# Kernel tuning notes

Measured on AMD Instinct MI355X. Metric: run time of the kernel, lower is better.

Reference implementation:

```python
import jax, jax.numpy as jnp
import numpy as np

def setup_inputs() -> dict:
    key = jax.random.key(0)
    kq, kk, kv = jax.random.split(key, 3)
    B, H, N, D = 2, 12, 4096, 64
    Q = jax.random.normal(kq, (B, H, N, D), dtype=jnp.float32)
    K = jax.random.normal(kk, (B, H, N, D), dtype=jnp.float32)
    V = jax.random.normal(kv, (B, H, N, D), dtype=jnp.float32)
    mask = jnp.ones((B, N), dtype=jnp.float32)
    return {"Q": Q, "K": K, "V": V, "mask": mask}

def reference(Q, K, V, mask):
    # Q, K, V: [B, H, N, D]; mask: [B, N]
    N = Q.shape[2]
    scale = 1.0 / jnp.sqrt(jnp.sqrt(jnp.float32(N)))  # N^(-1/4)
    m = mask[:, None, :, None]                         # [B,1,N,1]
    Qf = (jax.nn.elu(Q) + 1.0) * scale                 # feature map on queries
    Kf = (jax.nn.elu(K) + 1.0) * m * scale             # feature map + mask on keys
    Vm = V * m
    # linear attention: Q (K^T V), contracting over sequence first -> [B,H,D,D]
    KtV = jnp.einsum('bhnd,bhne->bhde', Kf, Vm)
    X = jnp.einsum('bhnd,bhde->bhne', Qf, KtV)
    return X
```

## Files before the change

kernel.cpp:

```cpp
#include <hip/hip_runtime.h>
#include <hip/hip_bf16.h>
#include <math.h>


#define BH_TOT 24
#define NROWS 4096
#define DD 64

typedef __attribute__((ext_vector_type(8))) short bf16x8;
typedef __attribute__((ext_vector_type(4))) float f32x4;

__device__ __forceinline__ float elu1(float x) {
    return x > 0.0f ? x + 1.0f : __expf(x);
}
__device__ __forceinline__ short f2bf(float x) {
    __hip_bfloat16 h = __float2bfloat16(x);
    return *reinterpret_cast<short*>(&h);
}

__global__ __launch_bounds__(128) void la_pass1(
        const float* __restrict__ K, const float* __restrict__ V,
        const float* __restrict__ mask, float* __restrict__ partial,
        float scale, int chunksPerWave) {
    const int bh   = blockIdx.x;
    const int slab = blockIdx.y;
    const int wave = threadIdx.x >> 6;
    const int lane = threadIdx.x & 63;
    const int g = lane >> 4, rg = g * 8, cl = lane & 15;

    const float* __restrict__ Kp = K + (size_t)bh * NROWS * DD;
    const float* __restrict__ Vp = V + (size_t)bh * NROWS * DD;
    const float* __restrict__ mp = mask + (size_t)(bh / 12) * NROWS;

    f32x4 acc[4][4];
#pragma unroll
    for (int i = 0; i < 4; ++i)
#pragma unroll
        for (int j = 0; j < 4; ++j) acc[i][j] = (f32x4)0.0f;

    const int rowsPerBlock = chunksPerWave * 64;
    const int n0 = slab * rowsPerBlock + wave * chunksPerWave * 32;

#pragma unroll 1
    for (int c = 0; c < chunksPerWave; ++c) {
        const int nb = n0 + c * 32 + rg;
        const float* kb = Kp + (size_t)nb * DD + cl;
        const float* vb = Vp + (size_t)nb * DD + cl;
        float mrow[8], kr[8][4], vr[8][4];
#pragma unroll
        for (int jj = 0; jj < 8; ++jj) {
            mrow[jj] = mp[nb + jj];
#pragma unroll
            for (int i = 0; i < 4; ++i) {
                kr[jj][i] = kb[jj * DD + i * 16];
                vr[jj][i] = vb[jj * DD + i * 16];
            }
        }
        bf16x8 af[4], bv[4];
#pragma unroll
        for (int i = 0; i < 4; ++i)
#pragma unroll
            for (int jj = 0; jj < 8; ++jj) {
                af[i][jj] = f2bf(elu1(kr[jj][i]) * (mrow[jj] * scale));
                bv[i][jj] = f2bf(vr[jj][i] * mrow[jj]);
            }
#pragma unroll
        for (int i = 0; i < 4; ++i)
#pragma unroll
            for (int j = 0; j < 4; ++j)
                acc[i][j] = __builtin_amdgcn_mfma_f32_16x16x32_bf16(
                                af[i], bv[j], acc[i][j], 0, 0, 0);
    }

    __shared__ float red[DD * 66];
#define RIDX(i, r, j) ((16 * (i) + 4 * g + (r)) * 66 + 16 * (j) + cl)
    if (wave == 1) {
#pragma unroll
        for (int i = 0; i < 4; ++i)
#pragma unroll
            for (int j = 0; j < 4; ++j)
#pragma unroll
                for (int r = 0; r < 4; ++r) red[RIDX(i, r, j)] = acc[i][j][r];
    }
    __syncthreads();
    if (wave == 0) {
        float* out = partial + ((size_t)bh * gridDim.y + slab) * (DD * DD);
#pragma unroll
        for (int i = 0; i < 4; ++i)
#pragma unroll
            for (int j = 0; j < 4; ++j)
#pragma unroll
                for (int r = 0; r < 4; ++r)
                    out[(16 * i + 4 * g + r) * DD + 16 * j + cl]
                        = acc[i][j][r] + red[RIDX(i, r, j)];
    }
#undef RIDX
}

__global__ __launch_bounds__(256) void la_pass2(
        const float* __restrict__ partial, __hip_bfloat16* __restrict__ ktvT,
        int nw) {
    const int bh = blockIdx.x;
    const int f4 = blockIdx.y * 256 + threadIdx.x;
    const f32x4* base = (const f32x4*)(partial + (size_t)bh * nw * DD * DD) + f4;
    f32x4 s = (f32x4)0.0f;
#pragma unroll 8
    for (int w = 0; w < nw; ++w)
        s += base[(size_t)w * (DD * DD / 4)];
    const int d = f4 >> 4, e0 = (f4 & 15) * 4;
    __hip_bfloat16* o = ktvT + (size_t)bh * DD * DD + d;
#pragma unroll
    for (int q = 0; q < 4; ++q)
        o[(size_t)(e0 + q) * DD] = __float2bfloat16(s[q]);
}

__global__ __launch_bounds__(256) void la_pass3(
        const float* __restrict__ Q, const __hip_bfloat16* __restrict__ ktvT,
        float* __restrict__ X, float scale) {
    const int bh   = blockIdx.x;
    const int wave = threadIdx.x >> 6;
    const int lane = threadIdx.x & 63;
    const int n0   = blockIdx.y * 128 + wave * 32;
    const int rg   = (lane >> 4) * 8;
    const int cl   = lane & 15;

    bf16x8 bfr[2][4];
#pragma unroll
    for (int c2 = 0; c2 < 2; ++c2)
#pragma unroll
        for (int j = 0; j < 4; ++j) {
            const __hip_bfloat16* p = ktvT + (size_t)bh * DD * DD
                                      + (size_t)(16 * j + cl) * DD + 32 * c2 + rg;
            bfr[c2][j] = *reinterpret_cast<const bf16x8*>(p);
        }

    const float* Qp = Q + (size_t)bh * NROWS * DD;
    bf16x8 afr[2][2];
#pragma unroll
    for (int i = 0; i < 2; ++i)
#pragma unroll
        for (int c2 = 0; c2 < 2; ++c2) {
            const float* qp = Qp + (size_t)(n0 + 16 * i + cl) * DD + 32 * c2 + rg;
            float4 q0 = ((const float4*)qp)[0];
            float4 q1 = ((const float4*)qp)[1];
            bf16x8 a;
            a[0] = f2bf(elu1(q0.x) * scale); a[1] = f2bf(elu1(q0.y) * scale);
            a[2] = f2bf(elu1(q0.z) * scale); a[3] = f2bf(elu1(q0.w) * scale);
            a[4] = f2bf(elu1(q1.x) * scale); a[5] = f2bf(elu1(q1.y) * scale);
            a[6] = f2bf(elu1(q1.z) * scale); a[7] = f2bf(elu1(q1.w) * scale);
            afr[i][c2] = a;
        }

    f32x4 acc[2][4];
#pragma unroll
    for (int i = 0; i < 2; ++i)
#pragma unroll
        for (int j = 0; j < 4; ++j) acc[i][j] = (f32x4)0.0f;

#pragma unroll
    for (int i = 0; i < 2; ++i)
#pragma unroll
        for (int j = 0; j < 4; ++j) {
            acc[i][j] = __builtin_amdgcn_mfma_f32_16x16x32_bf16(
                            afr[i][0], bfr[0][j], acc[i][j], 0, 0, 0);
            acc[i][j] = __builtin_amdgcn_mfma_f32_16x16x32_bf16(
                            afr[i][1], bfr[1][j], acc[i][j], 0, 0, 0);
        }

    float* Xp = X + (size_t)bh * NROWS * DD;
#pragma unroll
    for (int i = 0; i < 2; ++i)
#pragma unroll
        for (int j = 0; j < 4; ++j)
#pragma unroll
            for (int r = 0; r < 4; ++r)
                Xp[(size_t)(n0 + 16 * i + (lane >> 4) * 4 + r) * DD + 16 * j + cl]
                    = acc[i][j][r];
}

extern "C" void kernel_launch(void* const* d_in, const int* in_sizes, int n_in,
                              void* d_out, int out_size, void* d_ws, size_t ws_size,
                              hipStream_t stream) {
    const float* Q    = (const float*)d_in[0];
    const float* K    = (const float*)d_in[1];
    const float* V    = (const float*)d_in[2];
    const float* mask = (const float*)d_in[3];
    float* X = (float*)d_out;

    const float scale = 0.125f;

    int slabs = 32;
    while (slabs > 4 &&
           (size_t)BH_TOT * slabs * DD * DD * 4 + (size_t)BH_TOT * DD * DD * 2 > ws_size)
        slabs >>= 1;
    const int chunksPerWave = NROWS / (slabs * 64);

    float* partial = (float*)d_ws;
    __hip_bfloat16* ktvT =
        (__hip_bfloat16*)((char*)d_ws + (size_t)BH_TOT * slabs * DD * DD * 4);

    la_pass1<<<dim3(BH_TOT, slabs), 128, 0, stream>>>(K, V, mask, partial,
                                                      scale, chunksPerWave);
    la_pass2<<<dim3(BH_TOT, 4), 256, 0, stream>>>(partial, ktvT, slabs);
    la_pass3<<<dim3(BH_TOT, 32), 256, 0, stream>>>(Q, ktvT, X, scale);
}
```

Before: 34.23 us.

## Fuse partial reduction into pass1 via last-block atomic counter; vectorize pass3 stores

Merges the separate reduction kernel into the first pass: each block atomically bumps a per-head counter, and the last block to finish sums all slab partials and writes the bf16 K^T V matrix directly. It also swaps the MFMA operand order so the reduced matrix is stored transposed with vectorized writes, and pass3 is restructured so each lane stores contiguous float4 outputs. This removes one kernel launch but adds a memset, threadfences and a serialized tail reduction done by one block per head. The slab count is now fixed and no longer adapts to workspace size.

```diff
diff --git a/kernel.cpp b/kernel.cpp
--- a/kernel.cpp
+++ b/kernel.cpp
@@ -6,6 +6,7 @@
 #define BH_TOT 24
 #define NROWS 4096
 #define DD 64
+#define SLABS 32
 
 typedef __attribute__((ext_vector_type(8))) short bf16x8;
 typedef __attribute__((ext_vector_type(4))) float f32x4;
@@ -18,9 +19,10 @@
     return *reinterpret_cast<short*>(&h);
 }
 
-__global__ __launch_bounds__(128) void la_pass1(
+__global__ __launch_bounds__(128) void la_p12(
         const float* __restrict__ K, const float* __restrict__ V,
         const float* __restrict__ mask, float* __restrict__ partial,
+        __hip_bfloat16* __restrict__ ktvT, int* __restrict__ cnt,
         float scale, int chunksPerWave) {
     const int bh   = blockIdx.x;
     const int slab = blockIdx.y;
@@ -38,8 +40,7 @@
 #pragma unroll
         for (int j = 0; j < 4; ++j) acc[i][j] = (f32x4)0.0f;
 
-    const int rowsPerBlock = chunksPerWave * 64;
-    const int n0 = slab * rowsPerBlock + wave * chunksPerWave * 32;
+    const int n0 = slab * chunksPerWave * 64 + wave * chunksPerWave * 32;
 
 #pragma unroll 1
     for (int c = 0; c < chunksPerWave; ++c) {
@@ -65,82 +66,89 @@
                 bv[i][jj] = f2bf(vr[jj][i] * mrow[jj]);
             }
 #pragma unroll
-        for (int i = 0; i < 4; ++i)
-#pragma unroll
-            for (int j = 0; j < 4; ++j)
-                acc[i][j] = __builtin_amdgcn_mfma_f32_16x16x32_bf16(
-                                af[i], bv[j], acc[i][j], 0, 0, 0);
+        for (int je = 0; je < 4; ++je)
+#pragma unroll
+            for (int id = 0; id < 4; ++id)
+                acc[je][id] = __builtin_amdgcn_mfma_f32_16x16x32_bf16(
+                                  bv[je], af[id], acc[je][id], 0, 0, 0);
     }
 
     __shared__ float red[DD * 66];
-#define RIDX(i, r, j) ((16 * (i) + 4 * g + (r)) * 66 + 16 * (j) + cl)
+    __shared__ int lastFlag;
+#define RIDX(je, r, id) ((16 * (je) + 4 * g + (r)) * 66 + 16 * (id) + cl)
     if (wave == 1) {
 #pragma unroll
-        for (int i = 0; i < 4; ++i)
-#pragma unroll
-            for (int j = 0; j < 4; ++j)
-#pragma unroll
-                for (int r = 0; r < 4; ++r) red[RIDX(i, r, j)] = acc[i][j][r];
+        for (int je = 0; je < 4; ++je)
+#pragma unroll
+            for (int id = 0; id < 4; ++id)
+#pragma unroll
+                for (int r = 0; r < 4; ++r) red[RIDX(je, r, id)] = acc[je][id][r];
     }
     __syncthreads();
     if (wave == 0) {
-        float* out = partial + ((size_t)bh * gridDim.y + slab) * (DD * DD);
-#pragma unroll
-        for (int i = 0; i < 4; ++i)
-#pragma unroll
-            for (int j = 0; j < 4; ++j)
+        float* out = partial + ((size_t)bh * SLABS + slab) * (DD * DD);
+#pragma unroll
+        for (int je = 0; je < 4; ++je)
+#pragma unroll
+            for (int id = 0; id < 4; ++id)
 #pragma unroll
                 for (int r = 0; r < 4; ++r)
-                    out[(16 * i + 4 * g + r) * DD + 16 * j + cl]
-                        = acc[i][j][r] + red[RIDX(i, r, j)];
+                    out[(16 * je + 4 * g + r) * DD + 16 * id + cl]
+                        = acc[je][id][r] + red[RIDX(je, r, id)];
     }
 #undef RIDX
-}
-
-__global__ __launch_bounds__(256) void la_pass2(
-        const float* __restrict__ partial, __hip_bfloat16* __restrict__ ktvT,
-        int nw) {
-    const int bh = blockIdx.x;
-    const int f4 = blockIdx.y * 256 + threadIdx.x;
-    const f32x4* base = (const f32x4*)(partial + (size_t)bh * nw * DD * DD) + f4;
-    f32x4 s = (f32x4)0.0f;
+    __syncthreads();
+
+    if (threadIdx.x == 0) {
+        __threadfence();
+        int old = atomicAdd(&cnt[bh], 1);
+        lastFlag = (old == SLABS - 1) ? 1 : 0;
+    }
+    __syncthreads();
+    if (lastFlag) {
+        __threadfence();
+        const f32x4* base = (const f32x4*)(partial + (size_t)bh * SLABS * DD * DD);
+        __hip_bfloat16* ko = ktvT + (size_t)bh * DD * DD;
+#pragma unroll
+        for (int p = 0; p < 8; ++p) {
+            const int idx = threadIdx.x + p * 128;
+            f32x4 s = (f32x4)0.0f;
 #pragma unroll 8
-    for (int w = 0; w < nw; ++w)
-        s += base[(size_t)w * (DD * DD / 4)];
-    const int d = f4 >> 4, e0 = (f4 & 15) * 4;
-    __hip_bfloat16* o = ktvT + (size_t)bh * DD * DD + d;
-#pragma unroll
-    for (int q = 0; q < 4; ++q)
-        o[(size_t)(e0 + q) * DD] = __float2bfloat16(s[q]);
-}
-
-__global__ __launch_bounds__(256) void la_pass3(
+            for (int w = 0; w < SLABS; ++w)
+                s += base[(size_t)w * (DD * DD / 4) + idx];
+            const int e = idx >> 4, d0 = (idx & 15) * 4;
+            ushort4 u;
+            u.x = (unsigned short)f2bf(s[0]); u.y = (unsigned short)f2bf(s[1]);
+            u.z = (unsigned short)f2bf(s[2]); u.w = (unsigned short)f2bf(s[3]);
+            *reinterpret_cast<ushort4*>(ko + (size_t)e * DD + d0) = u;
+        }
+    }
+}
+
+__global__ __launch_bounds__(256) void la_p3(
         const float* __restrict__ Q, const __hip_bfloat16* __restrict__ ktvT,
         float* __restrict__ X, float scale) {
     const int bh   = blockIdx.x;
     const int wave = threadIdx.x >> 6;
     const int lane = threadIdx.x & 63;
     const int n0   = blockIdx.y * 128 + wave * 32;
-    const int rg   = (lane >> 4) * 8;
-    const int cl   = lane & 15;
-
-    bf16x8 bfr[2][4];
-#pragma unroll
-    for (int c2 = 0; c2 < 2; ++c2)
-#pragma unroll
-        for (int j = 0; j < 4; ++j) {
-            const __hip_bfloat16* p = ktvT + (size_t)bh * DD * DD
-                                      + (size_t)(16 * j + cl) * DD + 32 * c2 + rg;
-            bfr[c2][j] = *reinterpret_cast<const bf16x8*>(p);
-        }
+    const int g = lane >> 4, rg = g * 8, cl = lane & 15;
+
+    bf16x8 afr[4][2];
+#pragma unroll
+    for (int i = 0; i < 4; ++i)
+#pragma unroll
+        for (int c2 = 0; c2 < 2; ++c2)
+            afr[i][c2] = *reinterpret_cast<const bf16x8*>(
+                ktvT + (size_t)bh * DD * DD + (size_t)(16 * i + cl) * DD + 32 * c2 + rg);
 
     const float* Qp = Q + (size_t)bh * NROWS * DD;
-    bf16x8 afr[2][2];
-#pragma unroll
-    for (int i = 0; i < 2; ++i)
+    bf16x8 bfr[2][2];
+#pragma unroll
+    for (int t = 0; t < 2; ++t)
 #pragma unroll
         for (int c2 = 0; c2 < 2; ++c2) {
-            const float* qp = Qp + (size_t)(n0 + 16 * i + cl) * DD + 32 * c2 + rg;
+            const float* qp = Qp + (size_t)(n0 + 16 * t + cl) * DD + 32 * c2 + rg;
             float4 q0 = ((const float4*)qp)[0];
             float4 q1 = ((const float4*)qp)[1];
             bf16x8 a;
@@ -148,34 +156,35 @@
             a[2] = f2bf(elu1(q0.z) * scale); a[3] = f2bf(elu1(q0.w) * scale);
             a[4] = f2bf(elu1(q1.x) * scale); a[5] = f2bf(elu1(q1.y) * scale);
             a[6] = f2bf(elu1(q1.z) * scale); a[7] = f2bf(elu1(q1.w) * scale);
-            afr[i][c2] = a;
-        }
-
-    f32x4 acc[2][4];
-#pragma unroll
-    for (int i = 0; i < 2; ++i)
-#pragma unroll
-        for (int j = 0; j < 4; ++j) acc[i][j] = (f32x4)0.0f;
-
-#pragma unroll
-    for (int i = 0; i < 2; ++i)
-#pragma unroll
-        for (int j = 0; j < 4; ++j) {
-            acc[i][j] = __builtin_amdgcn_mfma_f32_16x16x32_bf16(
-                            afr[i][0], bfr[0][j], acc[i][j], 0, 0, 0);
-            acc[i][j] = __builtin_amdgcn_mfma_f32_16x16x32_bf16(
-                            afr[i][1], bfr[1][j], acc[i][j], 0, 0, 0);
+            bfr[t][c2] = a;
+        }
+
+    f32x4 acc[4][2];
+#pragma unroll
+    for (int i = 0; i < 4; ++i)
+#pragma unroll
+        for (int t = 0; t < 2; ++t) acc[i][t] = (f32x4)0.0f;
+
+#pragma unroll
+    for (int i = 0; i < 4; ++i)
+#pragma unroll
+        for (int t = 0; t < 2; ++t) {
+            acc[i][t] = __builtin_amdgcn_mfma_f32_16x16x32_bf16(
+                            afr[i][0], bfr[t][0], acc[i][t], 0, 0, 0);
+            acc[i][t] = __builtin_amdgcn_mfma_f32_16x16x32_bf16(
+                            afr[i][1], bfr[t][1], acc[i][t], 0, 0, 0);
         }
 
     float* Xp = X + (size_t)bh * NROWS * DD;
 #pragma unroll
-    for (int i = 0; i < 2; ++i)
-#pragma unroll
-        for (int j = 0; j < 4; ++j)
-#pragma unroll
-            for (int r = 0; r < 4; ++r)
-                Xp[(size_t)(n0 + 16 * i + (lane >> 4) * 4 + r) * DD + 16 * j + cl]
-                    = acc[i][j][r];
+    for (int i = 0; i < 4; ++i)
+#pragma unroll
+        for (int t = 0; t < 2; ++t) {
+            float4 v = make_float4(acc[i][t][0], acc[i][t][1],
+                                   acc[i][t][2], acc[i][t][3]);
+            *reinterpret_cast<float4*>(
+                Xp + (size_t)(n0 + 16 * t + cl) * DD + 16 * i + 4 * g) = v;
+        }
 }
 
 extern "C" void kernel_launch(void* const* d_in, const int* in_sizes, int n_in,
@@ -189,18 +198,14 @@
 
     const float scale = 0.125f;
 
-    int slabs = 32;
-    while (slabs > 4 &&
-           (size_t)BH_TOT * slabs * DD * DD * 4 + (size_t)BH_TOT * DD * DD * 2 > ws_size)
-        slabs >>= 1;
-    const int chunksPerWave = NROWS / (slabs * 64);
-
-    float* partial = (float*)d_ws;
-    __hip_bfloat16* ktvT =
-        (__hip_bfloat16*)((char*)d_ws + (size_t)BH_TOT * slabs * DD * DD * 4);
-
-    la_pass1<<<dim3(BH_TOT, slabs), 128, 0, stream>>>(K, V, mask, partial,
-                                                      scale, chunksPerWave);
-    la_pass2<<<dim3(BH_TOT, 4), 256, 0, stream>>>(partial, ktvT, slabs);
-    la_pass3<<<dim3(BH_TOT, 32), 256, 0, stream>>>(Q, ktvT, X, scale);
-}
+    int* cnt = (int*)d_ws;
+    __hip_bfloat16* ktvT = (__hip_bfloat16*)((char*)d_ws + 4096);
+    float* partial = (float*)((char*)d_ws + 4096 + (size_t)BH_TOT * DD * DD * 2);
+
+    const int chunksPerWave = NROWS / (SLABS * 64);
+
+    hipMemsetAsync(cnt, 0, BH_TOT * sizeof(int), stream);
+    la_p12<<<dim3(BH_TOT, SLABS), 128, 0, stream>>>(K, V, mask, partial, ktvT,
+                                                    cnt, scale, chunksPerWave);
+    la_p3<<<dim3(BH_TOT, 32), 256, 0, stream>>>(Q, ktvT, X, scale);
+}
```

Measured after the change: 74.64 us. 2.18x slower.
